# Performance work log

Hardware: AMD Instinct MI355X
Metric: run time of the kernel (lower is better)

Reference implementation:

```python
import jax, jax.numpy as jnp
import numpy as np

EPS = 1e-5

def layer_norm(x, w, b):
    mu = jnp.mean(x, axis=-1, keepdims=True)
    var = jnp.var(x, axis=-1, keepdims=True)
    return (x - mu) * jax.lax.rsqrt(var + EPS) * w + b

def setup_inputs() -> dict:
    key = jax.random.key(0)
    ks = jax.random.split(key, 9)
    B, N, d, hidden = 1, 512, 64, 128
    s = 0.02
    return {
        "z": jax.random.normal(ks[0], (B, N, N, d), dtype=jnp.float32),
        "ln_in_w": jnp.ones((d,), jnp.float32),
        "ln_in_b": jnp.zeros((d,), jnp.float32),
        "Wp": jax.random.normal(ks[1], (d, 2 * hidden), jnp.float32) * s,
        "Wg": jax.random.normal(ks[2], (d, 2 * hidden), jnp.float32) * s,
        "ln_out_w": jnp.ones((hidden,), jnp.float32),
        "ln_out_b": jnp.zeros((hidden,), jnp.float32),
        "Wout": jax.random.normal(ks[3], (hidden, d), jnp.float32) * s,
        "Wgate": jax.random.normal(ks[4], (d, d), jnp.float32) * s,
    }

def reference(z, ln_in_w, ln_in_b, Wp, Wg, ln_out_w, ln_out_b, Wout, Wgate):
    # z: [B, N, N, d]
    h = layer_norm(z, ln_in_w, ln_in_b)
    p = h @ Wp                               # [B,N,N,2*hidden]
    g_in = jax.nn.sigmoid(h @ Wg)            # [B,N,N,2*hidden]
    pg = p * g_in
    a, b = jnp.split(pg, 2, axis=-1)         # each [B,N,N,hidden]
    # direction == 'outgoing'
    out = jnp.einsum('bikd,bjkd->bijd', a, b)  # [B,N,N,hidden]
    out = layer_norm(out, ln_out_w, ln_out_b)
    g_out = jax.nn.sigmoid(h @ Wgate)        # [B,N,N,d]
    return (out @ Wout) * g_out              # [B,N,N,d]
```

## Files before the change

kernel.cpp:

```cpp
#include <hip/hip_runtime.h>
#include <hip/hip_fp16.h>


typedef _Float16 half_t;
typedef _Float16 f16x4 __attribute__((ext_vector_type(4)));
typedef _Float16 f16x8 __attribute__((ext_vector_type(8)));
typedef float f32x4 __attribute__((ext_vector_type(4)));

#define NSEQ 512
#define HID 128
#define ROWS (NSEQ * NSEQ)

#define GLOAD16(src, dst)                                                        \
    __builtin_amdgcn_global_load_lds(                                            \
        (const __attribute__((address_space(1))) void*)(src),                    \
        (__attribute__((address_space(3))) void*)(dst), 16, 0, 0)

__device__ __forceinline__ float fast_sigmoid(float x) {
    float e = __builtin_amdgcn_exp2f(-1.44269504088896f * x);
    return __builtin_amdgcn_rcpf(1.f + e);
}

__global__ void k_prep_w(const float* __restrict__ Wp, const float* __restrict__ Wg,
                         const float* __restrict__ Wgate,
                         const float* __restrict__ ln_out_w, const float* __restrict__ ln_out_b,
                         const float* __restrict__ Wout,
                         half_t* __restrict__ Wimg, half_t* __restrict__ W1t,
                         float* __restrict__ s1, float* __restrict__ s2) {
    int bid = blockIdx.x, t = threadIdx.x;
    if (bid < 18) {
        int chunk = bid * 256 + t;
        int ch = chunk >= 2304;
        int q = chunk - ch * 2304;
        int lr = q >> 3, slot = q & 7;
        int co = slot ^ (lr & 7);
        int grow;
        if (lr < 128)      grow = ch * 128 + lr;
        else if (lr < 256) grow = 256 + ch * 128 + (lr - 128);
        else               grow = 512 + ch * 32 + (lr - 256);
        f16x8 vals;
        #pragma unroll
        for (int j = 0; j < 8; ++j) {
            int l = co * 8 + j;
            float v;
            if (grow < 256)      v = Wp[l * 256 + grow];
            else if (grow < 512) v = Wg[l * 256 + (grow - 256)];
            else                 v = Wgate[l * 64 + (grow - 512)];
            vals[j] = (half_t)v;
        }
        *(f16x8*)(Wimg + (size_t)chunk * 8) = vals;
    } else {
        #pragma unroll
        for (int i = 0; i < 32; ++i) {
            int idx = t * 32 + i;
            int o = idx >> 7, c = idx & 127;
            W1t[idx] = (half_t)(ln_out_w[c] * Wout[c * 64 + o]);
        }
        if (t < 64) {
            float a1 = 0.f, a2 = 0.f;
            for (int c = 0; c < 128; ++c) {
                float wo = Wout[c * 64 + t];
                a1 += ln_out_w[c] * wo;
                a2 += ln_out_b[c] * wo;
            }
            s1[t] = a1; s2[t] = a2;
        }
    }
}

__global__ __launch_bounds__(256) void k_ln_in(const float* __restrict__ z,
                                               const float* __restrict__ w,
                                               const float* __restrict__ b,
                                               half_t* __restrict__ h) {
    int t = threadIdx.x;
    int row = blockIdx.x * 16 + (t >> 4);
    int c4 = t & 15;
    f32x4 x = *(const f32x4*)(z + (size_t)row * 64 + c4 * 4);
    float s = x[0] + x[1] + x[2] + x[3];
    float s2 = x[0]*x[0] + x[1]*x[1] + x[2]*x[2] + x[3]*x[3];
    #pragma unroll
    for (int off = 1; off < 16; off <<= 1) {
        s  += __shfl_xor(s,  off, 64);
        s2 += __shfl_xor(s2, off, 64);
    }
    float mu = s * (1.f / 64.f);
    float var = s2 * (1.f / 64.f) - mu * mu;
    float rs = rsqrtf(var + 1e-5f);
    f32x4 wv = *(const f32x4*)(w + c4 * 4);
    f32x4 bv = *(const f32x4*)(b + c4 * 4);
    f16x4 o;
    #pragma unroll
    for (int j = 0; j < 4; ++j)
        o[j] = (half_t)((x[j] - mu) * rs * wv[j] + bv[j]);
    *(f16x4*)(h + (size_t)row * 64 + c4 * 4) = o;
}

__global__ __launch_bounds__(256) void k_proj(const half_t* __restrict__ h,
                                              const half_t* __restrict__ Wimg,
                                              half_t* __restrict__ a_t,
                                              half_t* __restrict__ b_t,
                                              half_t* __restrict__ g_out) {
    __shared__ half_t Wl[288 * 64];
    __shared__ half_t pgl[64 * 66];

    int t = threadIdx.x;
    int ch = blockIdx.y;
    int bx = blockIdx.x;
    int r0 = bx * 64;
    int wid = t >> 6, lane = t & 63;
    int m = lane & 15, g = lane >> 4;

    const half_t* wsrc = Wimg + (size_t)ch * 2304 * 8;
    #pragma unroll
    for (int it = 0; it < 9; ++it) {
        int cb = it * 256 + wid * 64;
        GLOAD16(wsrc + (size_t)(cb + lane) * 8, Wl + (size_t)cb * 8);
    }

    int growbase = r0 + wid * 16;
    f16x8 af[2];
    #pragma unroll
    for (int ks = 0; ks < 2; ++ks)
        af[ks] = *(const f16x8*)(h + (size_t)(growbase + m) * 64 + ks * 32 + g * 8);

    __syncthreads();

    half_t* dst = (ch == 0) ? a_t : b_t;
    int swz = (bx >> 4) & 3;

    for (int grp = 0; grp < 2; ++grp) {
        #pragma unroll
        for (int pt4 = 0; pt4 < 4; ++pt4) {
            int pt = grp * 4 + pt4;
            f32x4 accp = {0.f, 0.f, 0.f, 0.f}, accg = {0.f, 0.f, 0.f, 0.f};
            #pragma unroll
            for (int ks = 0; ks < 2; ++ks) {
                int kb = (ks * 32 + g * 8) * 2;
                int lrp = pt * 16 + m;
                f16x8 bp = *(const f16x8*)((char*)Wl + lrp * 128 + (kb ^ ((lrp & 7) << 4)));
                int lrg = 128 + pt * 16 + m;
                f16x8 bg = *(const f16x8*)((char*)Wl + lrg * 128 + (kb ^ ((lrg & 7) << 4)));
                accp = __builtin_amdgcn_mfma_f32_16x16x32_f16(af[ks], bp, accp, 0, 0, 0);
                accg = __builtin_amdgcn_mfma_f32_16x16x32_f16(af[ks], bg, accg, 0, 0, 0);
            }
            f16x4 pk;
            #pragma unroll
            for (int r = 0; r < 4; ++r)
                pk[r] = (half_t)(accp[r] * fast_sigmoid(accg[r]));
            *(f16x4*)&pgl[(pt4 * 16 + m) * 66 + wid * 16 + g * 4] = pk;
        }
        __syncthreads();
        #pragma unroll
        for (int it = 0; it < 2; ++it) {
            int chunk = it * 256 + t;
            int cl = chunk >> 3, r8 = chunk & 7;
            f16x8 v = *(const f16x8*)&pgl[cl * 66 + r8 * 8];
            int dk = (r8 & 4) | ((r8 & 3) ^ swz);
            *(f16x8*)(dst + (size_t)(grp * 64 + cl) * ROWS + r0 + dk * 8) = v;
        }
        __syncthreads();
    }

    for (int gt = 0; gt < 2; ++gt) {
        f32x4 acc = {0.f, 0.f, 0.f, 0.f};
        #pragma unroll
        for (int ks = 0; ks < 2; ++ks) {
            int kb = (ks * 32 + g * 8) * 2;
            int lr = 256 + gt * 16 + m;
            f16x8 bb = *(const f16x8*)((char*)Wl + lr * 128 + (kb ^ ((lr & 7) << 4)));
            acc = __builtin_amdgcn_mfma_f32_16x16x32_f16(af[ks], bb, acc, 0, 0, 0);
        }
        int och = ch * 32 + gt * 16 + m;
        #pragma unroll
        for (int r = 0; r < 4; ++r) {
            float og = fast_sigmoid(acc[r]);
            int grow = growbase + g * 4 + r;
            g_out[(size_t)grow * 64 + och] = (half_t)og;
        }
    }
}

#define BUFH 12288
__global__ __launch_bounds__(256, 2) void k_einsum(const half_t* __restrict__ a_t,
                                                   const half_t* __restrict__ b_t,
                                                   half_t* __restrict__ out_mid) {
    __shared__ half_t lds[3 * BUFH];

    int t = threadIdx.x;
    int wid = t >> 6, lane = t & 63;
    int m = lane & 15, g = lane >> 4;

    int bid = blockIdx.x;
    int xcd = bid & 7;
    int idx = bid >> 3;
    int c = xcd + 8 * (idx >> 3);
    int tt = idx & 7;
    int i0 = (tt & 1) * 256, j0 = (tt >> 1) * 128;

    const half_t* A = a_t + (size_t)c * ROWS;
    const half_t* B = b_t + (size_t)c * ROWS;

    int wr = wid >> 1, wc = wid & 1;

    f32x4 acc[8][4] = {};

#define STAGE_A(ktt, base, it)                                                    \
    {                                                                             \
        int cb = (it) * 256 + wid * 64;              \
        int chunk = cb + lane;                                                    \
        GLOAD16(A + (size_t)(i0 + (chunk >> 2)) * 512 + (ktt) * 32 + (chunk & 3) * 8, \
                (base) + (size_t)cb * 8);                                         \
    }
#define STAGE_B(ktt, base, it)                                                    \
    {                                                                             \
        int cb = (it) * 256 + wid * 64;                                           \
        int chunk = cb + lane;                                                    \
        GLOAD16(B + (size_t)(j0 + (chunk >> 2)) * 512 + (ktt) * 32 + (chunk & 3) * 8, \
                (base) + 8192 + (size_t)cb * 8);                                  \
    }
#define STAGE_ALL(ktt, base)                                                      \
    STAGE_A(ktt, base, 0) STAGE_A(ktt, base, 1) STAGE_A(ktt, base, 2)             \
    STAGE_A(ktt, base, 3) STAGE_B(ktt, base, 0) STAGE_B(ktt, base, 1)

    STAGE_ALL(0, lds)
    STAGE_ALL(1, lds + BUFH)

    #pragma unroll
    for (int kt = 0; kt < 16; ++kt) {
        const half_t* Ac = lds + (kt % 3) * BUFH;
        const half_t* Bc = Ac + 8192;
        half_t* nxt = lds + ((kt + 2) % 3) * BUFH;

        if (kt <= 14) asm volatile("s_waitcnt vmcnt(6)" ::: "memory");
        else          asm volatile("s_waitcnt vmcnt(0)" ::: "memory");
        __builtin_amdgcn_s_barrier();
        __builtin_amdgcn_sched_barrier(0);

        f16x8 bf[4];
        #pragma unroll
        for (int ni = 0; ni < 4; ++ni) {
            int lrow = wc * 64 + ni * 16 + m;
            bf[ni] = *(const f16x8*)((const char*)Bc + lrow * 64 +
                                     ((g ^ ((lrow >> 1) & 3)) << 4));
        }

        #pragma unroll
        for (int q = 0; q < 4; ++q) {
            int lr0 = wr * 128 + (q * 2) * 16 + m;
            int lr1 = lr0 + 16;
            f16x8 af0 = *(const f16x8*)((const char*)Ac + lr0 * 64 +
                                        ((g ^ ((lr0 >> 1) & 3)) << 4));
            f16x8 af1 = *(const f16x8*)((const char*)Ac + lr1 * 64 +
                                        ((g ^ ((lr1 >> 1) & 3)) << 4));
            if (kt < 14) {
                if (q == 0)      { STAGE_A(kt + 2, nxt, 0) STAGE_A(kt + 2, nxt, 1) }
                else if (q == 1) { STAGE_A(kt + 2, nxt, 2) STAGE_A(kt + 2, nxt, 3) }
                else if (q == 2) { STAGE_B(kt + 2, nxt, 0) }
                else             { STAGE_B(kt + 2, nxt, 1) }
            }
            __builtin_amdgcn_s_setprio(1);
            #pragma unroll
            for (int ni = 0; ni < 4; ++ni) {
                acc[q * 2][ni]     = __builtin_amdgcn_mfma_f32_16x16x32_f16(af0, bf[ni], acc[q * 2][ni], 0, 0, 0);
                acc[q * 2 + 1][ni] = __builtin_amdgcn_mfma_f32_16x16x32_f16(af1, bf[ni], acc[q * 2 + 1][ni], 0, 0, 0);
            }
            __builtin_amdgcn_s_setprio(0);
        }
    }
#undef STAGE_ALL
#undef STAGE_B
#undef STAGE_A

    half_t* O = out_mid + (size_t)c * ROWS;
    #pragma unroll
    for (int mi = 0; mi < 8; ++mi) {
        #pragma unroll
        for (int ni = 0; ni < 4; ++ni) {
            int row = i0 + wr * 128 + mi * 16 + g * 4;
            int col = j0 + wc * 64 + ni * 16 + m;
            #pragma unroll
            for (int r2 = 0; r2 < 4; ++r2)
                O[(size_t)(row + r2) * 512 + col] = (half_t)acc[mi][ni][r2];
        }
    }
}

__global__ __launch_bounds__(256) void k_final(const half_t* __restrict__ out_mid,
                                               const half_t* __restrict__ W1t,
                                               const float* __restrict__ s1g,
                                               const float* __restrict__ s2g,
                                               const half_t* __restrict__ g_out,
                                               float* __restrict__ out) {
    __shared__ half_t midl[128 * 64];
    __shared__ half_t midt[64 * 128];
    __shared__ half_t w1l[64 * 128];
    __shared__ half_t gl[64 * 72];
    __shared__ float smu[64], srs[64], s1l[64], s2l[64];

    int t = threadIdx.x;
    int pos0 = blockIdx.x * 64;

    #pragma unroll
    for (int it = 0; it < 4; ++it) {
        int chunk = it * 256 + t;
        int cc = chunk >> 3, co = chunk & 7;
        *(uint4*)((char*)midl + cc * 128 + co * 16) =
            *(const uint4*)(out_mid + (size_t)cc * ROWS + pos0 + co * 8);
    }
    #pragma unroll
    for (int it = 0; it < 4; ++it) {
        int chunk = it * 256 + t;
        int row = chunk >> 4, slot = chunk & 15;
        *(uint4*)((char*)w1l + row * 256 + ((slot * 16) ^ ((row & 7) << 4))) =
            *(const uint4*)(W1t + row * 128 + slot * 8);
    }
    #pragma unroll
    for (int it = 0; it < 2; ++it) {
        int chunk = it * 256 + t;
        int row = chunk >> 3, co = chunk & 7;
        *(uint4*)((char*)gl + row * 144 + co * 16) =
            *(const uint4*)(g_out + (size_t)(pos0 + row) * 64 + co * 8);
    }
    if (t < 64) { s1l[t] = s1g[t]; s2l[t] = s2g[t]; }
    __syncthreads();

    {
        int p = t >> 2, q = t & 3;
        float s = 0.f, s2 = 0.f;
        #pragma unroll
        for (int cc4 = 0; cc4 < 4; ++cc4) {
            f16x8 pack;
            #pragma unroll
            for (int j = 0; j < 8; ++j) {
                half_t hv = midl[(q * 32 + cc4 * 8 + j) * 64 + p];
                float v = (float)hv;
                s += v; s2 += v * v;
                pack[j] = hv;
            }
            int slot = q * 4 + cc4;
            *(f16x8*)((char*)midt + p * 256 + ((slot * 16) ^ ((p & 7) << 4))) = pack;
        }
        s  += __shfl_xor(s, 1, 64);  s  += __shfl_xor(s, 2, 64);
        s2 += __shfl_xor(s2, 1, 64); s2 += __shfl_xor(s2, 2, 64);
        if (q == 0) {
            float mu = s * (1.f / 128.f);
            float var = s2 * (1.f / 128.f) - mu * mu;
            smu[p] = mu;
            srs[p] = rsqrtf(var + 1e-5f);
        }
    }
    __syncthreads();

    int wid = t >> 6, lane = t & 63;
    int m = lane & 15, g = lane >> 4;

    f32x4 acc[4] = {};
    #pragma unroll
    for (int ks = 0; ks < 4; ++ks) {
        int arow = wid * 16 + m;
        f16x8 af = *(const f16x8*)((char*)midt + arow * 256 +
                                   (((4 * ks + g) * 16) ^ ((arow & 7) << 4)));
        #pragma unroll
        for (int ni = 0; ni < 4; ++ni) {
            int brow = ni * 16 + m;
            f16x8 bf = *(const f16x8*)((char*)w1l + brow * 256 +
                                       (((4 * ks + g) * 16) ^ ((brow & 7) << 4)));
            acc[ni] = __builtin_amdgcn_mfma_f32_16x16x32_f16(af, bf, acc[ni], 0, 0, 0);
        }
    }

    #pragma unroll
    for (int ni = 0; ni < 4; ++ni) {
        int o = ni * 16 + m;
        float v1 = s1l[o], v2 = s2l[o];
        #pragma unroll
        for (int r = 0; r < 4; ++r) {
            int lrow = wid * 16 + g * 4 + r;
            float mu = smu[lrow], rs = srs[lrow];
            float val = acc[ni][r] * rs - mu * rs * v1 + v2;
            float gate = (float)gl[lrow * 72 + o];
            out[(size_t)(pos0 + lrow) * 64 + o] = val * gate;
        }
    }
}

extern "C" void kernel_launch(void* const* d_in, const int* in_sizes, int n_in,
                              void* d_out, int out_size, void* d_ws, size_t ws_size,
                              hipStream_t stream) {
    const float* z        = (const float*)d_in[0];
    const float* ln_in_w  = (const float*)d_in[1];
    const float* ln_in_b  = (const float*)d_in[2];
    const float* Wp       = (const float*)d_in[3];
    const float* Wg       = (const float*)d_in[4];
    const float* ln_out_w = (const float*)d_in[5];
    const float* ln_out_b = (const float*)d_in[6];
    const float* Wout     = (const float*)d_in[7];
    const float* Wgate    = (const float*)d_in[8];
    float* out = (float*)d_out;

    char* wsb = (char*)d_ws;
    half_t* Wimg = (half_t*)wsb;
    half_t* W1t  = (half_t*)(wsb + 81920);
    float*  s1   = (float*)(wsb + 98304);
    float*  s2   = (float*)(wsb + 98560);
    half_t* a_t  = (half_t*)(wsb + 131072);
    half_t* b_t  = a_t + (size_t)HID * ROWS;
    half_t* gout = b_t + (size_t)HID * ROWS;
    half_t* omid = gout + (size_t)ROWS * 64;
    half_t* h    = omid;

    k_prep_w<<<dim3(19), dim3(256), 0, stream>>>(Wp, Wg, Wgate, ln_out_w, ln_out_b, Wout,
                                                 Wimg, W1t, s1, s2);
    k_ln_in<<<dim3(ROWS / 16), dim3(256), 0, stream>>>(z, ln_in_w, ln_in_b, h);
    k_proj<<<dim3(ROWS / 64, 2), dim3(256), 0, stream>>>(h, Wimg, a_t, b_t, gout);
    k_einsum<<<dim3(1024), dim3(256), 0, stream>>>(a_t, b_t, omid);
    k_final<<<dim3(ROWS / 64), dim3(256), 0, stream>>>(omid, W1t, s1, s2, gout, out);
}
```

Before: 157.1 us.

## Halve einsum tile to 128x128 and double rows per projection block

The batched einsum kernel now uses 128x128 output tiles with smaller LDS buffers and a 4x4 accumulator per wave. The grid doubles to 2048 blocks with a new channel/tile mapping across XCDs, and the two-waves-per-SIMD launch bound is dropped. The projection kernel now processes 128 rows per block (two 64-row passes), so each block's weight load into LDS is reused over more rows and half as many blocks launch. The intent is better occupancy and load balance in the einsum, and amortized weight staging in the projection, at the cost of more global traffic per FLOP in the einsum.

After: 158.4 us. Within noise of the previous version (+0.8%).

```diff
diff --git a/kernel.cpp b/kernel.cpp
--- a/kernel.cpp
+++ b/kernel.cpp
@@ -106,7 +106,7 @@
     int t = threadIdx.x;
     int ch = blockIdx.y;
     int bx = blockIdx.x;
-    int r0 = bx * 64;
+    int r0 = bx * 128;
     int wid = t >> 6, lane = t & 63;
     int m = lane & 15, g = lane >> 4;
 
@@ -117,74 +117,81 @@
         GLOAD16(wsrc + (size_t)(cb + lane) * 8, Wl + (size_t)cb * 8);
     }
 
-    int growbase = r0 + wid * 16;
-    f16x8 af[2];
-    #pragma unroll
-    for (int ks = 0; ks < 2; ++ks)
-        af[ks] = *(const f16x8*)(h + (size_t)(growbase + m) * 64 + ks * 32 + g * 8);
+    f16x8 af[2][2];
+    #pragma unroll
+    for (int rp = 0; rp < 2; ++rp)
+        #pragma unroll
+        for (int ks = 0; ks < 2; ++ks)
+            af[rp][ks] = *(const f16x8*)(h + (size_t)(r0 + rp * 64 + wid * 16 + m) * 64
+                                           + ks * 32 + g * 8);
 
     __syncthreads();
 
     half_t* dst = (ch == 0) ? a_t : b_t;
-    int swz = (bx >> 4) & 3;
-
-    for (int grp = 0; grp < 2; ++grp) {
-        #pragma unroll
-        for (int pt4 = 0; pt4 < 4; ++pt4) {
-            int pt = grp * 4 + pt4;
-            f32x4 accp = {0.f, 0.f, 0.f, 0.f}, accg = {0.f, 0.f, 0.f, 0.f};
+    int swz = (bx >> 3) & 3;
+
+    #pragma unroll
+    for (int rp = 0; rp < 2; ++rp) {
+        int rbase = r0 + rp * 64;
+        for (int grp = 0; grp < 2; ++grp) {
+            #pragma unroll
+            for (int pt4 = 0; pt4 < 4; ++pt4) {
+                int pt = grp * 4 + pt4;
+                f32x4 accp = {0.f, 0.f, 0.f, 0.f}, accg = {0.f, 0.f, 0.f, 0.f};
+                #pragma unroll
+                for (int ks = 0; ks < 2; ++ks) {
+                    int kb = (ks * 32 + g * 8) * 2;
+                    int lrp = pt * 16 + m;
+                    f16x8 bp = *(const f16x8*)((char*)Wl + lrp * 128 + (kb ^ ((lrp & 7) << 4)));
+                    int lrg = 128 + pt * 16 + m;
+                    f16x8 bg = *(const f16x8*)((char*)Wl + lrg * 128 + (kb ^ ((lrg & 7) << 4)));
+                    accp = __builtin_amdgcn_mfma_f32_16x16x32_f16(af[rp][ks], bp, accp, 0, 0, 0);
+                    accg = __builtin_amdgcn_mfma_f32_16x16x32_f16(af[rp][ks], bg, accg, 0, 0, 0);
+                }
+                f16x4 pk;
+                #pragma unroll
+                for (int r = 0; r < 4; ++r)
+                    pk[r] = (half_t)(accp[r] * fast_sigmoid(accg[r]));
+                *(f16x4*)&pgl[(pt4 * 16 + m) * 66 + wid * 16 + g * 4] = pk;
+            }
+            __syncthreads();
+            #pragma unroll
+            for (int it = 0; it < 2; ++it) {
+                int chunk = it * 256 + t;
+                int cl = chunk >> 3, r8 = chunk & 7;
+                f16x8 v = *(const f16x8*)&pgl[cl * 66 + r8 * 8];
+                int dk = (r8 & 4) | ((r8 & 3) ^ swz);
+                *(f16x8*)(dst + (size_t)(grp * 64 + cl) * ROWS + rbase + dk * 8) = v;
+            }
+            __syncthreads();
+        }
+
+        #pragma unroll
+        for (int gt = 0; gt < 2; ++gt) {
+            f32x4 acc = {0.f, 0.f, 0.f, 0.f};
             #pragma unroll
             for (int ks = 0; ks < 2; ++ks) {
                 int kb = (ks * 32 + g * 8) * 2;
-                int lrp = pt * 16 + m;
-                f16x8 bp = *(const f16x8*)((char*)Wl + lrp * 128 + (kb ^ ((lrp & 7) << 4)));
-                int lrg = 128 + pt * 16 + m;
-                f16x8 bg = *(const f16x8*)((char*)Wl + lrg * 128 + (kb ^ ((lrg & 7) << 4)));
-                accp = __builtin_amdgcn_mfma_f32_16x16x32_f16(af[ks], bp, accp, 0, 0, 0);
-                accg = __builtin_amdgcn_mfma_f32_16x16x32_f16(af[ks], bg, accg, 0, 0, 0);
-            }
-            f16x4 pk;
-            #pragma unroll
-            for (int r = 0; r < 4; ++r)
-                pk[r] = (half_t)(accp[r] * fast_sigmoid(accg[r]));
-            *(f16x4*)&pgl[(pt4 * 16 + m) * 66 + wid * 16 + g * 4] = pk;
-        }
-        __syncthreads();
-        #pragma unroll
-        for (int it = 0; it < 2; ++it) {
-            int chunk = it * 256 + t;
-            int cl = chunk >> 3, r8 = chunk & 7;
-            f16x8 v = *(const f16x8*)&pgl[cl * 66 + r8 * 8];
-            int dk = (r8 & 4) | ((r8 & 3) ^ swz);
-            *(f16x8*)(dst + (size_t)(grp * 64 + cl) * ROWS + r0 + dk * 8) = v;
-        }
-        __syncthreads();
-    }
-
-    for (int gt = 0; gt < 2; ++gt) {
-        f32x4 acc = {0.f, 0.f, 0.f, 0.f};
-        #pragma unroll
-        for (int ks = 0; ks < 2; ++ks) {
-            int kb = (ks * 32 + g * 8) * 2;
-            int lr = 256 + gt * 16 + m;
-            f16x8 bb = *(const f16x8*)((char*)Wl + lr * 128 + (kb ^ ((lr & 7) << 4)));
-            acc = __builtin_amdgcn_mfma_f32_16x16x32_f16(af[ks], bb, acc, 0, 0, 0);
-        }
-        int och = ch * 32 + gt * 16 + m;
-        #pragma unroll
-        for (int r = 0; r < 4; ++r) {
-            float og = fast_sigmoid(acc[r]);
-            int grow = growbase + g * 4 + r;
-            g_out[(size_t)grow * 64 + och] = (half_t)og;
-        }
-    }
-}
-
-#define BUFH 12288
-__global__ __launch_bounds__(256, 2) void k_einsum(const half_t* __restrict__ a_t,
-                                                   const half_t* __restrict__ b_t,
-                                                   half_t* __restrict__ out_mid) {
-    __shared__ half_t lds[3 * BUFH];
+                int lr = 256 + gt * 16 + m;
+                f16x8 bb = *(const f16x8*)((char*)Wl + lr * 128 + (kb ^ ((lr & 7) << 4)));
+                acc = __builtin_amdgcn_mfma_f32_16x16x32_f16(af[rp][ks], bb, acc, 0, 0, 0);
+            }
+            int och = ch * 32 + gt * 16 + m;
+            #pragma unroll
+            for (int r = 0; r < 4; ++r) {
+                float og = fast_sigmoid(acc[r]);
+                int grow = rbase + wid * 16 + g * 4 + r;
+                g_out[(size_t)grow * 64 + och] = (half_t)og;
+            }
+        }
+    }
+}
+
+#define EBUF 8192
+__global__ __launch_bounds__(256) void k_einsum(const half_t* __restrict__ a_t,
+                                                const half_t* __restrict__ b_t,
+                                                half_t* __restrict__ out_mid) {
+    __shared__ half_t lds[3 * EBUF];
 
     int t = threadIdx.x;
     int wid = t >> 6, lane = t & 63;
@@ -192,17 +199,18 @@
 
     int bid = blockIdx.x;
     int xcd = bid & 7;
-    int idx = bid >> 3;
-    int c = xcd + 8 * (idx >> 3);
-    int tt = idx & 7;
-    int i0 = (tt & 1) * 256, j0 = (tt >> 1) * 128;
+    int rest = bid >> 3;
+    int gen = rest >> 6;
+    int local = rest & 63;
+    int c = xcd + 8 * (gen * 4 + (local >> 4));
+    int tile = local & 15;
+    int i0 = (tile >> 2) * 128, j0 = (tile & 3) * 128;
 
     const half_t* A = a_t + (size_t)c * ROWS;
     const half_t* B = b_t + (size_t)c * ROWS;
-
     int wr = wid >> 1, wc = wid & 1;
 
-    f32x4 acc[8][4] = {};
+    f32x4 acc[4][4] = {};
 
 #define STAGE_A(ktt, base, it)                                                    \
     {                                                                             \
@@ -216,22 +224,21 @@
         int cb = (it) * 256 + wid * 64;                                           \
         int chunk = cb + lane;                                                    \
         GLOAD16(B + (size_t)(j0 + (chunk >> 2)) * 512 + (ktt) * 32 + (chunk & 3) * 8, \
-                (base) + 8192 + (size_t)cb * 8);                                  \
+                (base) + 4096 + (size_t)cb * 8);                                  \
     }
 #define STAGE_ALL(ktt, base)                                                      \
-    STAGE_A(ktt, base, 0) STAGE_A(ktt, base, 1) STAGE_A(ktt, base, 2)             \
-    STAGE_A(ktt, base, 3) STAGE_B(ktt, base, 0) STAGE_B(ktt, base, 1)
+    STAGE_A(ktt, base, 0) STAGE_A(ktt, base, 1) STAGE_B(ktt, base, 0) STAGE_B(ktt, base, 1)
 
     STAGE_ALL(0, lds)
-    STAGE_ALL(1, lds + BUFH)
+    STAGE_ALL(1, lds + EBUF)
 
     #pragma unroll
     for (int kt = 0; kt < 16; ++kt) {
-        const half_t* Ac = lds + (kt % 3) * BUFH;
-        const half_t* Bc = Ac + 8192;
-        half_t* nxt = lds + ((kt + 2) % 3) * BUFH;
-
-        if (kt <= 14) asm volatile("s_waitcnt vmcnt(6)" ::: "memory");
+        const half_t* Ac = lds + (kt % 3) * EBUF;
+        const half_t* Bc = Ac + 4096;
+        half_t* nxt = lds + ((kt + 2) % 3) * EBUF;
+
+        if (kt <= 14) asm volatile("s_waitcnt vmcnt(4)" ::: "memory");
         else          asm volatile("s_waitcnt vmcnt(0)" ::: "memory");
         __builtin_amdgcn_s_barrier();
         __builtin_amdgcn_sched_barrier(0);
@@ -243,27 +250,21 @@
             bf[ni] = *(const f16x8*)((const char*)Bc + lrow * 64 +
                                      ((g ^ ((lrow >> 1) & 3)) << 4));
         }
-
-        #pragma unroll
-        for (int q = 0; q < 4; ++q) {
-            int lr0 = wr * 128 + (q * 2) * 16 + m;
-            int lr1 = lr0 + 16;
-            f16x8 af0 = *(const f16x8*)((const char*)Ac + lr0 * 64 +
-                                        ((g ^ ((lr0 >> 1) & 3)) << 4));
-            f16x8 af1 = *(const f16x8*)((const char*)Ac + lr1 * 64 +
-                                        ((g ^ ((lr1 >> 1) & 3)) << 4));
+        #pragma unroll
+        for (int mi = 0; mi < 4; ++mi) {
+            int lrow = wr * 64 + mi * 16 + m;
+            f16x8 afr = *(const f16x8*)((const char*)Ac + lrow * 64 +
+                                        ((g ^ ((lrow >> 1) & 3)) << 4));
             if (kt < 14) {
-                if (q == 0)      { STAGE_A(kt + 2, nxt, 0) STAGE_A(kt + 2, nxt, 1) }
-                else if (q == 1) { STAGE_A(kt + 2, nxt, 2) STAGE_A(kt + 2, nxt, 3) }
-                else if (q == 2) { STAGE_B(kt + 2, nxt, 0) }
-                else             { STAGE_B(kt + 2, nxt, 1) }
+                if (mi == 0)      STAGE_A(kt + 2, nxt, 0)
+                else if (mi == 1) STAGE_A(kt + 2, nxt, 1)
+                else if (mi == 2) STAGE_B(kt + 2, nxt, 0)
+                else              STAGE_B(kt + 2, nxt, 1)
             }
             __builtin_amdgcn_s_setprio(1);
             #pragma unroll
-            for (int ni = 0; ni < 4; ++ni) {
-                acc[q * 2][ni]     = __builtin_amdgcn_mfma_f32_16x16x32_f16(af0, bf[ni], acc[q * 2][ni], 0, 0, 0);
-                acc[q * 2 + 1][ni] = __builtin_amdgcn_mfma_f32_16x16x32_f16(af1, bf[ni], acc[q * 2 + 1][ni], 0, 0, 0);
-            }
+            for (int ni = 0; ni < 4; ++ni)
+                acc[mi][ni] = __builtin_amdgcn_mfma_f32_16x16x32_f16(afr, bf[ni], acc[mi][ni], 0, 0, 0);
             __builtin_amdgcn_s_setprio(0);
         }
     }
@@ -273,10 +274,10 @@
 
     half_t* O = out_mid + (size_t)c * ROWS;
     #pragma unroll
-    for (int mi = 0; mi < 8; ++mi) {
+    for (int mi = 0; mi < 4; ++mi) {
         #pragma unroll
         for (int ni = 0; ni < 4; ++ni) {
-            int row = i0 + wr * 128 + mi * 16 + g * 4;
+            int row = i0 + wr * 64 + mi * 16 + g * 4;
             int col = j0 + wc * 64 + ni * 16 + m;
             #pragma unroll
             for (int r2 = 0; r2 < 4; ++r2)
@@ -412,7 +413,7 @@
     k_prep_w<<<dim3(19), dim3(256), 0, stream>>>(Wp, Wg, Wgate, ln_out_w, ln_out_b, Wout,
                                                  Wimg, W1t, s1, s2);
     k_ln_in<<<dim3(ROWS / 16), dim3(256), 0, stream>>>(z, ln_in_w, ln_in_b, h);
-    k_proj<<<dim3(ROWS / 64, 2), dim3(256), 0, stream>>>(h, Wimg, a_t, b_t, gout);
-    k_einsum<<<dim3(1024), dim3(256), 0, stream>>>(a_t, b_t, omid);
+    k_proj<<<dim3(ROWS / 128, 2), dim3(256), 0, stream>>>(h, Wimg, a_t, b_t, gout);
+    k_einsum<<<dim3(2048), dim3(256), 0, stream>>>(a_t, b_t, omid);
     k_final<<<dim3(ROWS / 64), dim3(256), 0, stream>>>(omid, W1t, s1, s2, gout, out);
 }
```
